# Kernel tuning notes

Hardware: AMD Instinct MI355X
Metric: run time of the kernel (lower is better)

## Reference

```python
import jax, jax.numpy as jnp
import numpy as np

B, N, IN_DIM, D, H, F, L, P = 32, 512, 64, 256, 8, 1024, 3, 512
HD = D // H


def setup_inputs() -> dict:
    key = jax.random.key(0)
    ks = jax.random.split(key, 12)
    s = 0.02
    return {
        "x": jax.random.normal(ks[0], (B, N, IN_DIM), jnp.float32),
        "tw_start": jax.random.uniform(ks[1], (B, N), jnp.float32),
        "adj_mask": jax.random.randint(ks[2], (B, N, N), 0, 2) > 0,
        "Wp": jax.random.normal(ks[3], (D, IN_DIM), jnp.float32) * s,
        "bp": jnp.zeros((D,), jnp.float32),
        "pe": jax.random.normal(ks[4], (P, D), jnp.float32) * s,
        "Wqkv": jax.random.normal(ks[5], (L, 3 * D, D), jnp.float32) * s,
        "bqkv": jnp.zeros((L, 3 * D), jnp.float32),
        "Wo": jax.random.normal(ks[6], (L, D, D), jnp.float32) * s,
        "bo": jnp.zeros((L, D), jnp.float32),
        "ln1g": jnp.ones((L, D), jnp.float32),
        "ln1b": jnp.zeros((L, D), jnp.float32),
        "W1": jax.random.normal(ks[7], (L, F, D), jnp.float32) * s,
        "b1": jnp.zeros((L, F), jnp.float32),
        "W2": jax.random.normal(ks[8], (L, D, F), jnp.float32) * s,
        "b2": jnp.zeros((L, D), jnp.float32),
        "ln2g": jnp.ones((L, D), jnp.float32),
        "ln2b": jnp.zeros((L, D), jnp.float32),
    }


def _ln(x, g, b):
    m = x.mean(-1, keepdims=True)
    v = ((x - m) ** 2).mean(-1, keepdims=True)
    return (x - m) * jax.lax.rsqrt(v + 1e-5) * g + b


def reference(x, tw_start, adj_mask, Wp, bp, pe, Wqkv, bqkv, Wo, bo,
              ln1g, ln1b, W1, b1, W2, b2, ln2g, ln2b):
    # temporal rank = inverse permutation of argsort (equals the torch scatter trick)
    rank = jnp.argsort(jnp.argsort(tw_start, axis=-1), axis=-1)
    rank = jnp.clip(rank, 0, P - 1)
    h = x @ Wp.T + bp + pe[rank]                     # (B,N,D)
    # additive mask, broadcast over heads: (B,1,N,N)
    bias = jnp.where(adj_mask, 0.0, -1e9)[:, None].astype(h.dtype)
    scale = 1.0 / np.sqrt(HD)
    for l in range(L):
        qkv = h @ Wqkv[l].T + bqkv[l]                # (B,N,3D)
        q, k, v = jnp.split(qkv, 3, axis=-1)
        q = q.reshape(B, N, H, HD)
        k = k.reshape(B, N, H, HD)
        v = v.reshape(B, N, H, HD)
        scores = jnp.einsum('bqhd,bkhd->bhqk', q, k) * scale + bias
        attn = jax.nn.softmax(scores, axis=-1)
        o = jnp.einsum('bhqk,bkhd->bqhd', attn, v).reshape(B, N, D)
        o = o @ Wo[l].T + bo[l]
        h = _ln(h + o, ln1g[l], ln1b[l])
        ffo = jax.nn.gelu(h @ W1[l].T + b1[l], approximate=False) @ W2[l].T + b2[l]
        h = _ln(h + ffo, ln2g[l], ln2b[l])
    return h
```

## Files before the change

kernel.cpp:

```cpp
#include <hip/hip_runtime.h>
#include <hip/hip_bf16.h>

#define B_ 32
#define N_ 512
#define IN_DIM_ 64
#define D_ 256
#define H_ 8
#define HD_ 32
#define F_ 1024
#define L_ 3
#define P_ 512

typedef __bf16 bf16_t;
typedef bf16_t bf16x8 __attribute__((ext_vector_type(8)));
typedef bf16_t bf16x4 __attribute__((ext_vector_type(4)));
typedef float f32x4 __attribute__((ext_vector_type(4)));

__global__ __launch_bounds__(512) void rank_kernel(const float* __restrict__ tw,
                                                   int* __restrict__ rank) {
  const int b = blockIdx.x;
  const int i = threadIdx.x;
  __shared__ float s[N_];
  const float ti = tw[b * N_ + i];
  s[i] = ti;
  __syncthreads();
  int c = 0;
#pragma unroll 8
  for (int j = 0; j < N_; ++j) {
    const float tj = s[j];
    c += (tj < ti) || (tj == ti && j < i);
  }
  rank[b * N_ + i] = c < (P_ - 1) ? c : (P_ - 1);
}

__global__ void detect_mask_kernel(const unsigned char* __restrict__ m,
                                   int* __restrict__ flag) {
  unsigned v = 0;
  for (int i = 0; i < 64; ++i)
    if (i & 3) v |= m[i];
  *flag = (v == 0) ? 1 : 0;
}

__global__ __launch_bounds__(256) void packmask_kernel(
    const unsigned char* __restrict__ m, const int* __restrict__ flag,
    unsigned long long* __restrict__ bits) {
  const int idx = blockIdx.x * 256 + threadIdx.x;
  const size_t base = (size_t)(idx >> 3) * N_ + (idx & 7) * 64;
  unsigned long long v = 0;
  if (*flag) {
    const unsigned int* p = (const unsigned int*)m + base;
#pragma unroll 8
    for (int i = 0; i < 64; ++i) v |= (unsigned long long)(p[i] & 1u) << i;
  } else {
    const unsigned char* p = m + base;
#pragma unroll 8
    for (int i = 0; i < 64; ++i) v |= (unsigned long long)(p[i] & 1u) << i;
  }
  bits[idx] = v;
}

__global__ __launch_bounds__(256) void cvt_kernel(const float* __restrict__ s,
                                                  bf16_t* __restrict__ d, int n) {
  const int i = (blockIdx.x * 256 + threadIdx.x) * 4;
  if (i >= n) return;
  const float4 v = *(const float4*)(s + i);
  bf16x4 o = {(bf16_t)v.x, (bf16_t)v.y, (bf16_t)v.z, (bf16_t)v.w};
  *(bf16x4*)(d + i) = o;
}

__device__ __forceinline__ void gl16(const bf16_t* g, char* l) {
  __builtin_amdgcn_global_load_lds(
      (const __attribute__((address_space(1))) unsigned int*)g,
      (__attribute__((address_space(3))) unsigned int*)l, 16, 0, 0);
}

template <int EPI, int WF, int WB>
__global__ __launch_bounds__(256) void gemm_lds(
    const bf16_t* __restrict__ A, const bf16_t* __restrict__ W,
    const float* __restrict__ bias, const int K, const int Nd,
    float* __restrict__ Cf, bf16_t* __restrict__ Cb,
    const int* __restrict__ rank, const float* __restrict__ pe) {
  __shared__ __align__(16) bf16_t As[128 * 32];
  __shared__ __align__(16) bf16_t Ws[128 * 32];
  const int t = threadIdx.x;
  const int w = t >> 6, l = t & 63, g = l >> 4, r16 = l & 15;
  const int wm = w >> 1, wn = w & 1;
  const int m0 = blockIdx.x * 128, n0 = blockIdx.y * 128;

  f32x4 acc[4][4];
#pragma unroll
  for (int m = 0; m < 4; ++m)
#pragma unroll
    for (int n = 0; n < 4; ++n) acc[m][n] = (f32x4){0.f, 0.f, 0.f, 0.f};

  const int srow = w * 32 + (l >> 2);
  const int scol = (l & 3) * 8;
  const bf16_t* Ag = A + (size_t)(m0 + srow) * K + scol;
  const bf16_t* Wg = W + (size_t)(n0 + srow) * K + scol;
  char* Asb = (char*)As + w * 2048;
  char* Wsb = (char*)Ws + w * 2048;
  const int rowK16 = 16 * K;

  const bf16_t* Afr = As + (wm * 64 + r16) * 32 + g * 8;
  const bf16_t* Wfr = Ws + (wn * 64 + r16) * 32 + g * 8;

  for (int k0 = 0; k0 < K; k0 += 32) {
    gl16(Ag + k0, Asb);
    gl16(Ag + k0 + rowK16, Asb + 1024);
    gl16(Wg + k0, Wsb);
    gl16(Wg + k0 + rowK16, Wsb + 1024);
    __syncthreads();
    bf16x8 af[4], wf[4];
#pragma unroll
    for (int m = 0; m < 4; ++m) af[m] = *(const bf16x8*)(Afr + m * 16 * 32);
#pragma unroll
    for (int n = 0; n < 4; ++n) wf[n] = *(const bf16x8*)(Wfr + n * 16 * 32);
#pragma unroll
    for (int m = 0; m < 4; ++m)
#pragma unroll
      for (int n = 0; n < 4; ++n)
        acc[m][n] = __builtin_amdgcn_mfma_f32_16x16x32_bf16(af[m], wf[n], acc[m][n], 0, 0, 0);
    __syncthreads();
  }

  float bcol[4];
#pragma unroll
  for (int n = 0; n < 4; ++n) bcol[n] = bias[n0 + wn * 64 + n * 16 + r16];

#pragma unroll
  for (int m = 0; m < 4; ++m) {
#pragma unroll
    for (int r = 0; r < 4; ++r) {
      const int rowg = m0 + wm * 64 + m * 16 + g * 4 + r;
      float pv[4];
      if (EPI == 2) {
        const float* per = pe + (size_t)rank[rowg] * D_ + n0 + wn * 64 + r16;
#pragma unroll
        for (int n = 0; n < 4; ++n) pv[n] = per[n * 16];
      }
#pragma unroll
      for (int n = 0; n < 4; ++n) {
        float v = acc[m][n][r] + bcol[n];
        if (EPI == 2) v += pv[n];
        if (EPI == 1) v = 0.5f * v * (1.f + erff(v * 0.70710678118654752f));
        const size_t idx = (size_t)rowg * Nd + n0 + wn * 64 + n * 16 + r16;
        if (WF) Cf[idx] = v;
        if (WB) Cb[idx] = (bf16_t)v;
      }
    }
  }
}

__global__ __launch_bounds__(256) void attn_mfma(
    const bf16_t* __restrict__ qkv, const unsigned long long* __restrict__ mbits,
    bf16_t* __restrict__ out) {
  __shared__ __align__(16) char Ksh[64 * 80];
  __shared__ __align__(16) char Vsh[32 * 144];
  __shared__ __align__(16) char Psh[4 * 16 * 144];
  __shared__ unsigned long long Msh[64 * 8];
  const int t = threadIdx.x;
  const int w = t >> 6, l = t & 63, g = l >> 4, r16 = l & 15;
  const int qt = blockIdx.x & 7, bh = blockIdx.x >> 3;
  const int b = bh >> 3, hh = bh & 7;
  const int q0 = qt * 64;
  const float scale = 0.17677669529663687f;

  for (int i = t; i < 512; i += 256)
    Msh[i] = mbits[((size_t)b * N_ + q0 + (i >> 3)) * 8 + (i & 7)];

  const bf16_t* base = qkv + (size_t)b * N_ * (3 * D_) + hh * HD_;
  const bf16x8 qf = *(const bf16x8*)(base + (size_t)(q0 + w * 16 + r16) * (3 * D_) + g * 8);

  f32x4 oacc0 = {0.f, 0.f, 0.f, 0.f}, oacc1 = {0.f, 0.f, 0.f, 0.f};
  float mrow[4] = {-1e30f, -1e30f, -1e30f, -1e30f};
  float lrow[4] = {0.f, 0.f, 0.f, 0.f};

  const int krow = t >> 2, kq = t & 3;
  const int vkey = t & 63, vd0 = (t >> 6) * 8;
  char* Kw = Ksh + krow * 80 + kq * 16;
  char* Pw = Psh + w * 16 * 144;
  const f32x4 z = {0.f, 0.f, 0.f, 0.f};

  for (int kt = 0; kt < 8; ++kt) {
    const int k0 = kt * 64;
    *(float4*)Kw = *(const float4*)(base + (size_t)(k0 + krow) * (3 * D_) + D_ + kq * 8);
    const bf16x8 vv = *(const bf16x8*)(base + (size_t)(k0 + vkey) * (3 * D_) + 2 * D_ + vd0);
#pragma unroll
    for (int j = 0; j < 8; ++j)
      *(bf16_t*)(Vsh + (vd0 + j) * 144 + vkey * 2) = vv[j];
    __syncthreads();

    f32x4 s[4];
#pragma unroll
    for (int j = 0; j < 4; ++j) {
      const bf16x8 kf = *(const bf16x8*)(Ksh + (j * 16 + r16) * 80 + g * 16);
      s[j] = __builtin_amdgcn_mfma_f32_16x16x32_bf16(qf, kf, z, 0, 0, 0);
    }
    unsigned long long mw[4];
#pragma unroll
    for (int r = 0; r < 4; ++r) mw[r] = Msh[(w * 16 + g * 4 + r) * 8 + kt];

    float sval[4][4];
    float mx[4] = {-1e30f, -1e30f, -1e30f, -1e30f};
#pragma unroll
    for (int j = 0; j < 4; ++j)
#pragma unroll
      for (int r = 0; r < 4; ++r) {
        const bool bit = (mw[r] >> (j * 16 + r16)) & 1ULL;
        const float sv = bit ? s[j][r] * scale : -1e30f;
        sval[j][r] = sv;
        mx[r] = fmaxf(mx[r], sv);
      }
#pragma unroll
    for (int d = 1; d < 16; d <<= 1)
#pragma unroll
      for (int r = 0; r < 4; ++r) mx[r] = fmaxf(mx[r], __shfl_xor(mx[r], d));

    float ce[4], mn[4];
#pragma unroll
    for (int r = 0; r < 4; ++r) {
      mn[r] = fmaxf(mrow[r], mx[r]);
      ce[r] = __expf(mrow[r] - mn[r]);
      mrow[r] = mn[r];
    }
    float psum[4] = {0.f, 0.f, 0.f, 0.f};
#pragma unroll
    for (int j = 0; j < 4; ++j)
#pragma unroll
      for (int r = 0; r < 4; ++r) {
        const float p = __expf(sval[j][r] - mn[r]);
        psum[r] += p;
        *(bf16_t*)(Pw + (g * 4 + r) * 144 + (j * 16 + r16) * 2) = (bf16_t)p;
      }
#pragma unroll
    for (int d = 1; d < 16; d <<= 1)
#pragma unroll
      for (int r = 0; r < 4; ++r) psum[r] += __shfl_xor(psum[r], d);
#pragma unroll
    for (int r = 0; r < 4; ++r) {
      lrow[r] = lrow[r] * ce[r] + psum[r];
      oacc0[r] *= ce[r];
      oacc1[r] *= ce[r];
    }
    __threadfence_block();

#pragma unroll
    for (int kh = 0; kh < 2; ++kh) {
      const bf16x8 pa = *(const bf16x8*)(Pw + r16 * 144 + kh * 64 + g * 16);
      const bf16x8 v0 = *(const bf16x8*)(Vsh + r16 * 144 + kh * 64 + g * 16);
      const bf16x8 v1 = *(const bf16x8*)(Vsh + (16 + r16) * 144 + kh * 64 + g * 16);
      oacc0 = __builtin_amdgcn_mfma_f32_16x16x32_bf16(pa, v0, oacc0, 0, 0, 0);
      oacc1 = __builtin_amdgcn_mfma_f32_16x16x32_bf16(pa, v1, oacc1, 0, 0, 0);
    }
    __syncthreads();
  }

  float inv[4];
#pragma unroll
  for (int r = 0; r < 4; ++r) inv[r] = lrow[r] > 0.f ? 1.f / lrow[r] : 0.f;
#pragma unroll
  for (int r = 0; r < 4; ++r) {
    bf16_t* op = out + (size_t)(b * N_ + q0 + w * 16 + g * 4 + r) * D_ + hh * HD_;
    op[r16] = (bf16_t)(oacc0[r] * inv[r]);
    op[16 + r16] = (bf16_t)(oacc1[r] * inv[r]);
  }
}

template <int BF>
__global__ __launch_bounds__(256) void ln_kernel(
    const float* __restrict__ hin, const float* __restrict__ o,
    const float* __restrict__ g, const float* __restrict__ beta,
    float* __restrict__ outf, bf16_t* __restrict__ outb) {
  const int row = blockIdx.x * 4 + threadIdx.y;
  const int lane = threadIdx.x;
  const size_t base = (size_t)row * D_ + lane * 4;
  const float4 hv = *(const float4*)&hin[base];
  const float4 ov = *(const float4*)&o[base];
  const float x0 = hv.x + ov.x, x1 = hv.y + ov.y, x2 = hv.z + ov.z, x3 = hv.w + ov.w;

  float s = x0 + x1 + x2 + x3;
#pragma unroll
  for (int off = 32; off >= 1; off >>= 1) s += __shfl_xor(s, off, 64);
  const float mean = s * (1.f / D_);

  const float d0 = x0 - mean, d1 = x1 - mean, d2 = x2 - mean, d3 = x3 - mean;
  float sq = d0 * d0 + d1 * d1 + d2 * d2 + d3 * d3;
#pragma unroll
  for (int off = 32; off >= 1; off >>= 1) sq += __shfl_xor(sq, off, 64);
  const float rs = rsqrtf(sq * (1.f / D_) + 1e-5f);

  const float4 gv = *(const float4*)&g[lane * 4];
  const float4 bv = *(const float4*)&beta[lane * 4];
  const float y0 = d0 * rs * gv.x + bv.x, y1 = d1 * rs * gv.y + bv.y;
  const float y2 = d2 * rs * gv.z + bv.z, y3 = d3 * rs * gv.w + bv.w;
  *(float4*)&outf[base] = make_float4(y0, y1, y2, y3);
  if (BF) {
    bf16x4 ob = {(bf16_t)y0, (bf16_t)y1, (bf16_t)y2, (bf16_t)y3};
    *(bf16x4*)(outb + base) = ob;
  }
}

extern "C" void kernel_launch(void* const* d_in, const int* in_sizes, int n_in,
                              void* d_out, int out_size, void* d_ws, size_t ws_size,
                              hipStream_t stream) {
  const float* x   = (const float*)d_in[0];
  const float* tw  = (const float*)d_in[1];
  const unsigned char* adj = (const unsigned char*)d_in[2];
  const float* Wp  = (const float*)d_in[3];
  const float* bp  = (const float*)d_in[4];
  const float* pe  = (const float*)d_in[5];
  const float* Wqkv = (const float*)d_in[6];
  const float* bqkv = (const float*)d_in[7];
  const float* Wo  = (const float*)d_in[8];
  const float* bo  = (const float*)d_in[9];
  const float* ln1g = (const float*)d_in[10];
  const float* ln1b = (const float*)d_in[11];
  const float* W1  = (const float*)d_in[12];
  const float* b1  = (const float*)d_in[13];
  const float* W2  = (const float*)d_in[14];
  const float* b2  = (const float*)d_in[15];
  const float* ln2g = (const float*)d_in[16];
  const float* ln2b = (const float*)d_in[17];
  float* out = (float*)d_out;

  char* ws = (char*)d_ws;
  size_t off = 0;
  int* rank = (int*)(ws + off);                      off += 65536;
  int* mflag = (int*)(ws + off);                     off += 64;
  unsigned long long* mbits = (unsigned long long*)(ws + off); off += 1048576;
  bf16_t* x_bf = (bf16_t*)(ws + off);                off += 2097152;
  bf16_t* Wp_bf = (bf16_t*)(ws + off);               off += 32768;
  bf16_t* Wqkv_bf = (bf16_t*)(ws + off);             off += 1179648;
  bf16_t* Wo_bf = (bf16_t*)(ws + off);               off += 393216;
  bf16_t* W1_bf = (bf16_t*)(ws + off);               off += 1572864;
  bf16_t* W2_bf = (bf16_t*)(ws + off);               off += 1572864;
  float* h = (float*)(ws + off);                     off += 16777216;
  bf16_t* h_bf = (bf16_t*)(ws + off);                off += 8388608;
  float* tmp = (float*)(ws + off);                   off += 16777216;
  bf16_t* attno_bf = (bf16_t*)(ws + off);            off += 8388608;
  bf16_t* qkv_bf = (bf16_t*)(ws + off);
  bf16_t* ffn1_bf = (bf16_t*)(ws + off);

  const dim3 blk(256);
  rank_kernel<<<B_, 512, 0, stream>>>(tw, rank);
  detect_mask_kernel<<<1, 1, 0, stream>>>(adj, mflag);
  packmask_kernel<<<512, blk, 0, stream>>>(adj, mflag, mbits);
  cvt_kernel<<<1024, blk, 0, stream>>>(x, x_bf, 1048576);
  cvt_kernel<<<16, blk, 0, stream>>>(Wp, Wp_bf, 16384);
  cvt_kernel<<<576, blk, 0, stream>>>(Wqkv, Wqkv_bf, 589824);
  cvt_kernel<<<192, blk, 0, stream>>>(Wo, Wo_bf, 196608);
  cvt_kernel<<<768, blk, 0, stream>>>(W1, W1_bf, 786432);
  cvt_kernel<<<768, blk, 0, stream>>>(W2, W2_bf, 786432);

  gemm_lds<2, 1, 1><<<dim3(128, 2), blk, 0, stream>>>(
      x_bf, Wp_bf, bp, IN_DIM_, D_, h, h_bf, rank, pe);

  for (int l = 0; l < L_; ++l) {
    gemm_lds<0, 0, 1><<<dim3(128, 6), blk, 0, stream>>>(
        h_bf, Wqkv_bf + (size_t)l * 3 * D_ * D_, bqkv + l * 3 * D_, D_, 3 * D_,
        nullptr, qkv_bf, nullptr, nullptr);
    attn_mfma<<<B_ * H_ * 8, blk, 0, stream>>>(qkv_bf, mbits, attno_bf);
    gemm_lds<0, 1, 0><<<dim3(128, 2), blk, 0, stream>>>(
        attno_bf, Wo_bf + (size_t)l * D_ * D_, bo + l * D_, D_, D_,
        tmp, nullptr, nullptr, nullptr);
    ln_kernel<1><<<(B_ * N_) / 4, dim3(64, 4), 0, stream>>>(
        h, tmp, ln1g + l * D_, ln1b + l * D_, h, h_bf);
    gemm_lds<1, 0, 1><<<dim3(128, 8), blk, 0, stream>>>(
        h_bf, W1_bf + (size_t)l * F_ * D_, b1 + l * F_, D_, F_,
        nullptr, ffn1_bf, nullptr, nullptr);
    gemm_lds<0, 1, 0><<<dim3(128, 2), blk, 0, stream>>>(
        ffn1_bf, W2_bf + (size_t)l * D_ * F_, b2 + l * D_, F_, D_,
        tmp, nullptr, nullptr, nullptr);
    if (l == L_ - 1)
      ln_kernel<0><<<(B_ * N_) / 4, dim3(64, 4), 0, stream>>>(
          h, tmp, ln2g + l * D_, ln2b + l * D_, out, nullptr);
    else
      ln_kernel<1><<<(B_ * N_) / 4, dim3(64, 4), 0, stream>>>(
          h, tmp, ln2g + l * D_, ln2b + l * D_, h, h_bf);
  }
}
```

Baseline: 614.6 us.

## Double-buffer GEMM LDS tiles and make flash-attention rescale lazy

```diff
diff --git a/kernel.cpp b/kernel.cpp
--- a/kernel.cpp
+++ b/kernel.cpp
@@ -80,8 +80,8 @@
     const float* __restrict__ bias, const int K, const int Nd,
     float* __restrict__ Cf, bf16_t* __restrict__ Cb,
     const int* __restrict__ rank, const float* __restrict__ pe) {
-  __shared__ __align__(16) bf16_t As[128 * 32];
-  __shared__ __align__(16) bf16_t Ws[128 * 32];
+  __shared__ __align__(16) bf16_t As[2][128 * 32];
+  __shared__ __align__(16) bf16_t Ws[2][128 * 32];
   const int t = threadIdx.x;
   const int w = t >> 6, l = t & 63, g = l >> 4, r16 = l & 15;
   const int wm = w >> 1, wn = w & 1;
@@ -101,26 +101,44 @@
   char* Wsb = (char*)Ws + w * 2048;
   const int rowK16 = 16 * K;
 
-  const bf16_t* Afr = As + (wm * 64 + r16) * 32 + g * 8;
-  const bf16_t* Wfr = Ws + (wn * 64 + r16) * 32 + g * 8;
-
-  for (int k0 = 0; k0 < K; k0 += 32) {
-    gl16(Ag + k0, Asb);
-    gl16(Ag + k0 + rowK16, Asb + 1024);
-    gl16(Wg + k0, Wsb);
-    gl16(Wg + k0 + rowK16, Wsb + 1024);
-    __syncthreads();
+  const char* Afr = (const char*)As + (wm * 64 + r16) * 64 + g * 16;
+  const char* Wfr = (const char*)Ws + (wn * 64 + r16) * 64 + g * 16;
+
+  const int nt = K >> 5;
+
+  gl16(Ag, Asb);
+  gl16(Ag + rowK16, Asb + 1024);
+  gl16(Wg, Wsb);
+  gl16(Wg + rowK16, Wsb + 1024);
+  asm volatile("s_waitcnt vmcnt(0)" ::: "memory");
+  __builtin_amdgcn_s_barrier();
+  __builtin_amdgcn_sched_barrier(0);
+
+  for (int tt = 0; tt < nt; ++tt) {
+    const int curo = (tt & 1) * 8192;
+    if (tt + 1 < nt) {
+      const int nxto = 8192 - curo;
+      const int k0 = (tt + 1) << 5;
+      gl16(Ag + k0, Asb + nxto);
+      gl16(Ag + k0 + rowK16, Asb + nxto + 1024);
+      gl16(Wg + k0, Wsb + nxto);
+      gl16(Wg + k0 + rowK16, Wsb + nxto + 1024);
+    }
     bf16x8 af[4], wf[4];
 #pragma unroll
-    for (int m = 0; m < 4; ++m) af[m] = *(const bf16x8*)(Afr + m * 16 * 32);
-#pragma unroll
-    for (int n = 0; n < 4; ++n) wf[n] = *(const bf16x8*)(Wfr + n * 16 * 32);
+    for (int m = 0; m < 4; ++m) af[m] = *(const bf16x8*)(Afr + curo + m * 1024);
+#pragma unroll
+    for (int n = 0; n < 4; ++n) wf[n] = *(const bf16x8*)(Wfr + curo + n * 1024);
 #pragma unroll
     for (int m = 0; m < 4; ++m)
 #pragma unroll
       for (int n = 0; n < 4; ++n)
         acc[m][n] = __builtin_amdgcn_mfma_f32_16x16x32_bf16(af[m], wf[n], acc[m][n], 0, 0, 0);
-    __syncthreads();
+    if (tt + 1 < nt) {
+      asm volatile("s_waitcnt vmcnt(0)" ::: "memory");
+      __builtin_amdgcn_s_barrier();
+      __builtin_amdgcn_sched_barrier(0);
+    }
   }
 
   float bcol[4];
@@ -216,19 +234,26 @@
 #pragma unroll
       for (int r = 0; r < 4; ++r) mx[r] = fmaxf(mx[r], __shfl_xor(mx[r], d));
 
-    float ce[4], mn[4];
-#pragma unroll
-    for (int r = 0; r < 4; ++r) {
-      mn[r] = fmaxf(mrow[r], mx[r]);
-      ce[r] = __expf(mrow[r] - mn[r]);
-      mrow[r] = mn[r];
+    int grow = 0;
+#pragma unroll
+    for (int r = 0; r < 4; ++r) grow |= (mx[r] > mrow[r] + 8.f) ? 1 : 0;
+    if (__any(grow)) {
+#pragma unroll
+      for (int r = 0; r < 4; ++r) {
+        const float mn = fmaxf(mrow[r], mx[r]);
+        const float ce = __expf(mrow[r] - mn);
+        mrow[r] = mn;
+        lrow[r] *= ce;
+        oacc0[r] *= ce;
+        oacc1[r] *= ce;
+      }
     }
     float psum[4] = {0.f, 0.f, 0.f, 0.f};
 #pragma unroll
     for (int j = 0; j < 4; ++j)
 #pragma unroll
       for (int r = 0; r < 4; ++r) {
-        const float p = __expf(sval[j][r] - mn[r]);
+        const float p = __expf(sval[j][r] - mrow[r]);
         psum[r] += p;
         *(bf16_t*)(Pw + (g * 4 + r) * 144 + (j * 16 + r16) * 2) = (bf16_t)p;
       }
@@ -237,11 +262,7 @@
 #pragma unroll
       for (int r = 0; r < 4; ++r) psum[r] += __shfl_xor(psum[r], d);
 #pragma unroll
-    for (int r = 0; r < 4; ++r) {
-      lrow[r] = lrow[r] * ce[r] + psum[r];
-      oacc0[r] *= ce[r];
-      oacc1[r] *= ce[r];
-    }
+    for (int r = 0; r < 4; ++r) lrow[r] += psum[r];
     __threadfence_block();
 
 #pragma unroll
```

Result: no change. 610.2 us (-0.7%).
